# Performance work log

Hardware: AMD Instinct MI355X
Metric: run time of the kernel (lower is better)

The kernel has to match this reference:

```python
import math
import jax, jax.numpy as jnp
import numpy as np

N_NODES = 4096
N_EDGES = 16384
N_EFEAT = 16384
L = 8          # mem_token
DIM = 512
HEAD = 8
NL = 2         # mid_num_layers
ROPE_THETA = 10000.0


def _rms(x, w, eps=1e-6):
    v = jnp.mean(jnp.square(x), axis=-1, keepdims=True)
    return x * jax.lax.rsqrt(v + eps) * w


def _rope_cos_sin(seq_len, d, theta):
    inv = 1.0 / (theta ** (jnp.arange(0, d, 2, dtype=jnp.float32) / d))
    f = jnp.outer(jnp.arange(seq_len, dtype=jnp.float32), inv)  # [L, d/2]
    emb = jnp.concatenate([f, f], axis=-1)                       # [L, d]
    return jnp.cos(emb), jnp.sin(emb)


def _rot_half(x):
    h = x.shape[-1] // 2
    return jnp.concatenate([-x[..., h:], x[..., :h]], axis=-1)


def setup_inputs() -> dict:
    key = jax.random.key(0)
    ks = jax.random.split(key, 12)
    s = 0.02
    return {
        "hidden_states": jax.random.normal(ks[0], (N_NODES + N_EFEAT, L * DIM), jnp.float32),
        "edge_index": jax.random.randint(ks[1], (2, N_EDGES), 0, N_NODES),
        "edge_map": jax.random.randint(ks[2], (N_EDGES,), 0, N_EFEAT),
        "num_node_feat": N_NODES,
        "W_qkv": jax.random.normal(ks[3], (NL, DIM, 3 * DIM), jnp.float32) * s,
        "W_e": jax.random.normal(ks[4], (NL, DIM, 2 * DIM), jnp.float32) * s,
        "W_o": jax.random.normal(ks[5], (NL, DIM, DIM), jnp.float32) * s,
        "x_norm_w": jnp.ones((NL, DIM), jnp.float32),
        "xe_norm_w": jnp.ones((NL, DIM), jnp.float32),
        "post_norm_w": jnp.ones((NL, DIM), jnp.float32),
        "ff_W1": jax.random.normal(ks[6], (NL, DIM, 2 * DIM), jnp.float32) * s,
        "ff_b1": jnp.zeros((NL, 2 * DIM), jnp.float32),
        "ff_W2": jax.random.normal(ks[7], (NL, 2 * DIM, DIM), jnp.float32) * s,
        "ff_b2": jnp.zeros((NL, DIM), jnp.float32),
    }


def reference(hidden_states, edge_index, edge_map, num_node_feat,
              W_qkv, W_e, W_o, x_norm_w, xe_norm_w, post_norm_w,
              ff_W1, ff_b1, ff_W2, ff_b2):
    n_layers, dim = W_qkv.shape[0], W_qkv.shape[1]
    n_tot = hidden_states.shape[0]
    seq = hidden_states.shape[1] // dim           # mem_token
    d = dim // HEAD                               # d_model per head
    N = int(num_node_feat)
    src, dst = edge_index[0], edge_index[1]
    cos, sin = _rope_cos_sin(seq, d, ROPE_THETA)
    cos = cos[None, :, None, :]   # [1, L, 1, d]
    sin = sin[None, :, None, :]
    inv_sqrt_d = 1.0 / math.sqrt(d)

    h = hidden_states.reshape(n_tot, seq, dim)
    for l in range(n_layers):
        x = h[:N]                        # [N, L, dim]
        xe = h[N:][edge_map]             # [E, L, dim]
        res = x
        xn = _rms(x, x_norm_w[l])
        xen = _rms(xe, xe_norm_w[l])
        q, k, v = jnp.split(jnp.einsum('nld,de->nle', xn, W_qkv[l]), 3, axis=-1)
        ek, ev = jnp.split(jnp.einsum('eld,df->elf', xen, W_e[l]), 2, axis=-1)
        # gather per-edge, fuse edge features into key/value
        qi = q[dst].reshape(-1, seq, HEAD, d)
        kj = (k[src] + ek).reshape(-1, seq, HEAD, d)
        vj = (v[src] + ev).reshape(-1, seq, HEAD, d)
        # rotary over memory-token positions
        qi = qi * cos + _rot_half(qi) * sin
        kj = kj * cos + _rot_half(kj) * sin
        alpha = jnp.einsum('elhd,elhd->elh', qi, kj) * inv_sqrt_d  # [E, L, H]
        # segment softmax over incoming edges of each destination node
        m = jax.ops.segment_max(alpha, dst, num_segments=N)
        m = jnp.where(jnp.isfinite(m), m, 0.0)
        a = jnp.exp(alpha - m[dst])
        s = jax.ops.segment_sum(a, dst, num_segments=N)
        a = a / (s[dst] + 1e-16)
        out_e = (vj * a[..., None]).reshape(-1, seq, dim)          # [E, L, dim]
        agg = jax.ops.segment_sum(out_e, dst, num_segments=N)      # [N, L, dim]
        out = res + jnp.einsum('nld,de->nle', agg, W_o[l])
        res2 = out
        o = _rms(out, post_norm_w[l])
        ff = jnp.einsum('nlf,fd->nld',
                        jax.nn.relu(jnp.einsum('nld,df->nlf', o, ff_W1[l]) + ff_b1[l]),
                        ff_W2[l]) + ff_b2[l]
        out = res2 + ff
        h = jnp.concatenate([out, h[N:]], axis=0)
    return h
```

## Files before the change

kernel.cpp:

```cpp
#include <hip/hip_runtime.h>

typedef unsigned short u16;
typedef unsigned int   u32;
typedef u16   u16x8 __attribute__((ext_vector_type(8)));
typedef __bf16 bf16x8 __attribute__((ext_vector_type(8)));
typedef float f32x4 __attribute__((ext_vector_type(4)));
typedef float f32x4v __attribute__((ext_vector_type(4)));

#define N_NODES 4096
#define N_EDGES 16384
#define N_EFEAT 16384
#define SEQ 8
#define DIM 512
#define NLAYER 2
#define NROWS_X (N_NODES*SEQ)
#define NROWS_E (N_EDGES*SEQ)

__device__ __forceinline__ float b2f(u16 u){ return __uint_as_float(((u32)u)<<16); }
__device__ __forceinline__ u16 f2b(float f){ u32 b=__float_as_uint(f); b += 0x7FFFu + ((b>>16)&1u); return (u16)(b>>16); }

__device__ __forceinline__ void gl16(const u16* g, u16* l) {
    __builtin_amdgcn_global_load_lds((const __attribute__((address_space(1))) void*)g,
                                     (__attribute__((address_space(3))) void*)l, 16, 0, 0);
}

#define TF_SEG(CNT, SRC, DST, FOLD, KK, NN)                                   \
    if (b < (CNT)) {                                                          \
        int idx = b * 256 + threadIdx.x;                                      \
        int c = idx / (NN), j = idx - c * (NN);                               \
        float v = (SRC)[idx];                                                 \
        if (FOLD) v *= (FOLD)[c];                                             \
        (DST)[(size_t)j * (KK) + c] = f2b(v);                                 \
        return;                                                               \
    }                                                                         \
    b -= (CNT);

__global__ void k_tfall(const float* __restrict__ Wqkv, const float* __restrict__ We,
                        const float* __restrict__ Wo,   const float* __restrict__ W1,
                        const float* __restrict__ W2,
                        const float* __restrict__ xw, const float* __restrict__ xew,
                        const float* __restrict__ pw,
                        u16* __restrict__ WtQKV, u16* __restrict__ WtE, u16* __restrict__ WtO,
                        u16* __restrict__ Wt1, u16* __restrict__ Wt2,
                        float* __restrict__ z0, float* __restrict__ z1,
                        float* __restrict__ z2, int* __restrict__ zf)
{
    int b = blockIdx.x;
    if (b >= 20480) {
        b -= 20480;
        if (b < 128) { z0[b * 256 + threadIdx.x] = 0.f; return; }
        b -= 128;
        if (b < 128) { z1[b * 256 + threadIdx.x] = 0.f; return; }
        b -= 128;
        if (b < 128) { z2[b * 256 + threadIdx.x] = 0.f; return; }
        b -= 128;
        zf[b * 256 + threadIdx.x] = 0; return;
    }
    int l = b / 10240; b -= l * 10240;
    TF_SEG(3072, Wqkv + (size_t)l*512*1536, WtQKV + (size_t)l*1536*512, xw  + l*512, 512, 1536)
    TF_SEG(2048, We   + (size_t)l*512*1024, WtE   + (size_t)l*1024*512, xew + l*512, 512, 1024)
    TF_SEG(1024, Wo   + (size_t)l*512*512,  WtO   + (size_t)l*512*512,  (const float*)nullptr, 512, 512)
    TF_SEG(2048, W1   + (size_t)l*512*1024, Wt1   + (size_t)l*1024*512, pw  + l*512, 512, 1024)
    TF_SEG(2048, W2   + (size_t)l*1024*512, Wt2   + (size_t)l*512*1024, (const float*)nullptr, 1024, 512)
}

__global__ void k_prep(const float* __restrict__ hidden, const int* __restrict__ ulist,
                       const int* __restrict__ ucnt,
                       u16* __restrict__ fbf, float* __restrict__ s_f,
                       u16* __restrict__ hb, float* __restrict__ ssx0)
{
    int lane = threadIdx.x & 63;
    const float* p;
    u16* dst; float* ssout; int orow;
    if (blockIdx.x < NROWS_E / 4) {
        int fr = blockIdx.x * 4 + (threadIdx.x >> 6);
        if (fr >= ucnt[0] * SEQ) return;
        int j = fr >> 3, l = fr & 7;
        p = hidden + ((size_t)(N_NODES + ulist[j]) * SEQ + l) * DIM;
        dst = fbf + (size_t)fr * DIM; ssout = s_f; orow = fr;
    } else {
        int row = (blockIdx.x - NROWS_E / 4) * 4 + (threadIdx.x >> 6);
        p = hidden + (size_t)row * DIM;
        dst = hb + (size_t)row * DIM; ssout = ssx0; orow = row;
    }
    f32x4v v0 = *(const f32x4v*)(p + lane * 8);
    f32x4v v1 = *(const f32x4v*)(p + lane * 8 + 4);
    float ss = v0[0]*v0[0]+v0[1]*v0[1]+v0[2]*v0[2]+v0[3]*v0[3]
             + v1[0]*v1[0]+v1[1]*v1[1]+v1[2]*v1[2]+v1[3]*v1[3];
    #pragma unroll
    for (int d = 1; d < 64; d <<= 1) ss += __shfl_xor(ss, d);
    if (lane == 0) ssout[orow] = ss;
    u16x8 o;
    #pragma unroll
    for (int i = 0; i < 4; ++i) o[i] = f2b(v0[i]);
    #pragma unroll
    for (int i = 0; i < 4; ++i) o[4+i] = f2b(v1[i]);
    *(u16x8*)(dst + lane * 8) = o;
}

__global__ void k_mark(const int* __restrict__ emap, int* __restrict__ flag)
{
    int e = blockIdx.x * 256 + threadIdx.x;
    if (e < N_EDGES) flag[emap[e]] = 1;
}
__global__ void k_scanf(const int* __restrict__ flag, int* __restrict__ newid,
                        int* __restrict__ ulist, int* __restrict__ ucnt)
{
    __shared__ int part[256];
    int t = threadIdx.x;
    int base = t * 64;
    int loc[64]; int s = 0;
    #pragma unroll
    for (int i = 0; i < 64; ++i) { loc[i] = s; s += flag[base + i]; }
    part[t] = s; __syncthreads();
    for (int d = 1; d < 256; d <<= 1) {
        int v = (t >= d) ? part[t - d] : 0;
        __syncthreads();
        part[t] += v;
        __syncthreads();
    }
    int pre = (t == 0) ? 0 : part[t - 1];
    #pragma unroll
    for (int i = 0; i < 64; ++i) {
        int m = base + i;
        int id = pre + loc[i];
        newid[m] = id;
        if (flag[m]) ulist[id] = m;
    }
    if (t == 255) ucnt[0] = part[255];
}
__global__ void k_fidx(const int* __restrict__ emap, const int* __restrict__ newid,
                       int* __restrict__ fidx)
{
    int e = blockIdx.x * 256 + threadIdx.x;
    if (e < N_EDGES) fidx[e] = newid[emap[e]];
}

__global__ void k_count(const int* __restrict__ dstA, int* __restrict__ cnt)
{
    int e = blockIdx.x * 256 + threadIdx.x;
    if (e < N_EDGES) atomicAdd(&cnt[dstA[e]], 1);
}
__global__ void k_scan(const int* __restrict__ cnt, int* __restrict__ off)
{
    __shared__ int part[256];
    int t = threadIdx.x;
    int base = t * 16;
    int loc[16]; int s = 0;
    #pragma unroll
    for (int i = 0; i < 16; ++i) { loc[i] = s; s += cnt[base + i]; }
    part[t] = s; __syncthreads();
    for (int d = 1; d < 256; d <<= 1) {
        int v = (t >= d) ? part[t - d] : 0;
        __syncthreads();
        part[t] += v;
        __syncthreads();
    }
    int pre = (t == 0) ? 0 : part[t - 1];
    #pragma unroll
    for (int i = 0; i < 16; ++i) off[base + i] = pre + loc[i];
    if (t == 255) off[N_NODES] = part[255];
}
__global__ void k_fill(const int* __restrict__ dstA, const int* __restrict__ off,
                       int* __restrict__ cur, int* __restrict__ elist)
{
    int e = blockIdx.x * 256 + threadIdx.x;
    if (e < N_EDGES) {
        int d = dstA[e];
        int pos = off[d] + atomicAdd(&cur[d], 1);
        elist[pos] = e;
    }
}

#define GEMM_BODY(BID, A_, B_, N_, K_, GX_, MROWS_, SSIN_, BIAS_, RELU_, RESH_, SSOUT_, OUTF_, OUTH_) \
{                                                                                   \
    int tid  = threadIdx.x;                                                         \
    int lane = tid & 63, wid = tid >> 6;                                            \
    int xcd  = (BID) & 7;                                                           \
    int ii_  = (BID) >> 3;                                                          \
    int colt = ii_ % (GX_);                                                         \
    int rowt = (ii_ / (GX_)) * 8 + xcd;                                             \
    int row0 = rowt * 128, col0 = colt * 128;                                       \
    if ((MROWS_) && row0 >= (MROWS_)[0] * SEQ) return;                              \
    int r0 = wid * 32 + (lane >> 2);                                                \
    int r1 = r0 + 16;                                                               \
    int ce0 = ((lane & 3) * 8) ^ (((r0 >> 1) & 3) << 3);                            \
    int ce1 = ((lane & 3) * 8) ^ (((r1 >> 1) & 3) << 3);                            \
    const u16* ga0 = (A_) + (size_t)(row0 + r0) * (K_) + ce0;                       \
    const u16* ga1 = (A_) + (size_t)(row0 + r1) * (K_) + ce1;                       \
    const u16* gb0 = (B_) + (size_t)(col0 + r0) * (K_) + ce0;                       \
    const u16* gb1 = (B_) + (size_t)(col0 + r1) * (K_) + ce1;                       \
    f32x4 acc[4][4];                                                                \
    _Pragma("unroll")                                                               \
    for (int m = 0; m < 4; ++m)                                                     \
        _Pragma("unroll")                                                           \
        for (int n = 0; n < 4; ++n) { f32x4 z = {0.f,0.f,0.f,0.f}; acc[m][n] = z; } \
    int wr = wid >> 1, wc = wid & 1;                                                \
    int m15 = lane & 15, g = lane >> 4;                                             \
    int arow_l = wr * 64 + m15;                                                     \
    int brow_l = wc * 64 + m15;                                                     \
    int ksw = (g * 8) ^ (((m15 >> 1) & 3) << 3);                                    \
    int NT = (K_) / 32;                                                             \
    {                                                                               \
        gl16(ga0, &ldsA[0][wid * 1024]);                                            \
        gl16(ga1, &ldsA[0][wid * 1024 + 512]);                                      \
        gl16(gb0, &ldsB[0][wid * 1024]);                                            \
        gl16(gb1, &ldsB[0][wid * 1024 + 512]);                                      \
    }                                                                               \
    int cur = 0;                                                                    \
    for (int kt = 0; kt < NT; ++kt) {                                               \
        __syncthreads();                                                            \
        if (kt + 1 < NT) {                                                          \
            int ko = (kt + 1) * 32, bf_ = cur ^ 1;                                  \
            gl16(ga0 + ko, &ldsA[bf_][wid * 1024]);                                 \
            gl16(ga1 + ko, &ldsA[bf_][wid * 1024 + 512]);                           \
            gl16(gb0 + ko, &ldsB[bf_][wid * 1024]);                                 \
            gl16(gb1 + ko, &ldsB[bf_][wid * 1024 + 512]);                           \
        }                                                                           \
        bf16x8 af[4], bfr[4];                                                       \
        _Pragma("unroll")                                                           \
        for (int m = 0; m < 4; ++m)                                                 \
            af[m] = *(const bf16x8*)&ldsA[cur][(arow_l + m * 16) * 32 + ksw];       \
        _Pragma("unroll")                                                           \
        for (int n = 0; n < 4; ++n)                                                 \
            bfr[n] = *(const bf16x8*)&ldsB[cur][(brow_l + n * 16) * 32 + ksw];      \
        _Pragma("unroll")                                                           \
        for (int m = 0; m < 4; ++m)                                                 \
            _Pragma("unroll")                                                       \
            for (int n = 0; n < 4; ++n)                                             \
                acc[m][n] = __builtin_amdgcn_mfma_f32_16x16x32_bf16(af[m], bfr[n], acc[m][n], 0, 0, 0); \
        cur ^= 1;                                                                   \
    }                                                                               \
    _Pragma("unroll")                                                               \
    for (int m = 0; m < 4; ++m) {                                                   \
        _Pragma("unroll")                                                           \
        for (int j = 0; j < 4; ++j) {                                               \
            int row = row0 + wr * 64 + m * 16 + g * 4 + j;                          \
            float sc = 0.f;                                                         \
            if (SSIN_) sc = rsqrtf((SSIN_)[row] * (1.f / (float)DIM) + 1e-6f);      \
            float ssa = 0.f;                                                        \
            _Pragma("unroll")                                                       \
            for (int n = 0; n < 4; ++n) {                                           \
                int col = col0 + wc * 64 + n * 16 + m15;                            \
                float v = acc[m][n][j];                                             \
                if (SSIN_) v *= sc;                                                 \
                if (BIAS_) v += (BIAS_)[col];                                       \
                if (RELU_) v = fmaxf(v, 0.f);                                       \
                if (RESH_) v += b2f((RESH_)[(size_t)row * (N_) + col]);             \
                if (OUTF_) (OUTF_)[(size_t)row * (N_) + col] = v;                   \
                if (OUTH_) (OUTH_)[(size_t)row * (N_) + col] = f2b(v);              \
                ssa += v * v;                                                       \
            }                                                                       \
            if (SSOUT_) {                                                           \
                ssa += __shfl_xor(ssa, 1);                                          \
                ssa += __shfl_xor(ssa, 2);                                          \
                ssa += __shfl_xor(ssa, 4);                                          \
                ssa += __shfl_xor(ssa, 8);                                          \
                if (m15 == 0) atomicAdd(&(SSOUT_)[row], ssa);                       \
            }                                                                       \
        }                                                                           \
    }                                                                               \
}

__global__ __launch_bounds__(256, 2) void k_gemm(
    const u16* __restrict__ A, const u16* __restrict__ B,
    int M, int N, int K, int gx, const int* __restrict__ mrows,
    const float* __restrict__ ssin, const float* __restrict__ bias, int relu,
    const u16* __restrict__ resH, float* __restrict__ ssout,
    float* __restrict__ outF, u16* __restrict__ outH)
{
    __shared__ u16 ldsA[2][128 * 32];
    __shared__ u16 ldsB[2][128 * 32];
    GEMM_BODY(blockIdx.x, A, B, N, K, gx, mrows, ssin, bias, relu, resH, ssout, outF, outH)
}

__global__ __launch_bounds__(256, 2) void k_gemm2(
    int nb0,
    const u16* __restrict__ A0, const u16* __restrict__ B0,
    int N0, int K0, int gx0, const int* __restrict__ mrows0,
    const float* __restrict__ ssin0, const float* __restrict__ bias0, int relu0,
    const u16* __restrict__ resH0, float* __restrict__ ssout0,
    float* __restrict__ outF0, u16* __restrict__ outH0,
    const u16* __restrict__ A1, const u16* __restrict__ B1,
    int N1, int K1, int gx1, const int* __restrict__ mrows1,
    const float* __restrict__ ssin1, const float* __restrict__ bias1, int relu1,
    const u16* __restrict__ resH1, float* __restrict__ ssout1,
    float* __restrict__ outF1, u16* __restrict__ outH1)
{
    __shared__ u16 ldsA[2][128 * 32];
    __shared__ u16 ldsB[2][128 * 32];
    if ((int)blockIdx.x < nb0) {
        GEMM_BODY(blockIdx.x, A0, B0, N0, K0, gx0, mrows0, ssin0, bias0, relu0, resH0, ssout0, outF0, outH0)
    } else {
        int bid = blockIdx.x - nb0;
        GEMM_BODY(bid, A1, B1, N1, K1, gx1, mrows1, ssin1, bias1, relu1, resH1, ssout1, outF1, outH1)
    }
}

__global__ __launch_bounds__(256, 2) void k_gemm_copy(
    int nb0,
    const u16* __restrict__ A, const u16* __restrict__ B,
    int N, int K, int gx,
    const float* __restrict__ ssin, const float* __restrict__ bias, int relu,
    const u16* __restrict__ resH, float* __restrict__ ssout,
    float* __restrict__ outF, u16* __restrict__ outH,
    const f32x4v* __restrict__ csrc, f32x4v* __restrict__ cdst)
{
    __shared__ u16 ldsA[2][128 * 32];
    __shared__ u16 ldsB[2][128 * 32];
    if ((int)blockIdx.x < nb0) {
        GEMM_BODY(blockIdx.x, A, B, N, K, gx, (const int*)nullptr, ssin, bias, relu, resH, ssout, outF, outH)
    } else {
        size_t t = (size_t)(blockIdx.x - nb0) * 256 + threadIdx.x;
        #pragma unroll
        for (int k = 0; k < 32; ++k)
            cdst[t + (size_t)k * 524288] = csrc[t + (size_t)k * 524288];
    }
}

__global__ __launch_bounds__(256, 2) void k_attn(
    const u16* __restrict__ qkv, const u16* __restrict__ ekv,
    const int* __restrict__ srcA, const int* __restrict__ fidx,
    const int* __restrict__ off, const int* __restrict__ elist,
    u16* __restrict__ agg)
{
    int n = blockIdx.x;
    int t = threadIdx.x;
    int pair = t >> 2, sub = t & 3;
    int l = pair >> 3, hd = pair & 7;
    int doff = hd * 64 + sub * 16;

    size_t qrow = ((size_t)n * SEQ + l) * 1536;
    float qi[16];
    {
        u16x8 qa = *(const u16x8*)&qkv[qrow + doff];
        u16x8 qb = *(const u16x8*)&qkv[qrow + doff + 8];
        #pragma unroll
        for (int i = 0; i < 8; ++i) { qi[i] = b2f(qa[i]); qi[i + 8] = b2f(qb[i]); }
    }

    float mrun = -INFINITY, s = 0.f;
    float av[16];
    #pragma unroll
    for (int i = 0; i < 16; ++i) av[i] = 0.f;

    int e0 = off[n], e1 = off[n + 1];
    for (int ii = e0; ii < e1; ++ii) {
        int e = elist[ii];
        int es = srcA[e];
        size_t krow = ((size_t)es * SEQ + l) * 1536 + 512;
        size_t erow = ((size_t)fidx[e] * SEQ + l) * 1024;

        u16x8 ka = *(const u16x8*)&qkv[krow + doff];
        u16x8 kb = *(const u16x8*)&qkv[krow + doff + 8];
        u16x8 ea = *(const u16x8*)&ekv[erow + doff];
        u16x8 eb = *(const u16x8*)&ekv[erow + doff + 8];

        float dot = 0.f;
        #pragma unroll
        for (int i = 0; i < 8; ++i) {
            dot += qi[i]     * (b2f(ka[i]) + b2f(ea[i]));
            dot += qi[i + 8] * (b2f(kb[i]) + b2f(eb[i]));
        }
        dot += __shfl_xor(dot, 1);
        dot += __shfl_xor(dot, 2);
        float alpha = dot * 0.125f;

        float mn = fmaxf(mrun, alpha);
        float f = expf(mrun - mn);
        float p = expf(alpha - mn);
        s = s * f + p;

        u16x8 va  = *(const u16x8*)&qkv[krow + 512 + doff];
        u16x8 vb  = *(const u16x8*)&qkv[krow + 512 + doff + 8];
        u16x8 eva = *(const u16x8*)&ekv[erow + 512 + doff];
        u16x8 evb = *(const u16x8*)&ekv[erow + 512 + doff + 8];
        #pragma unroll
        for (int i = 0; i < 8; ++i) {
            av[i]     = av[i]     * f + p * (b2f(va[i]) + b2f(eva[i]));
            av[i + 8] = av[i + 8] * f + p * (b2f(vb[i]) + b2f(evb[i]));
        }
        mrun = mn;
    }

    float inv = 1.f / (s + 1e-16f);
    size_t orow = ((size_t)n * SEQ + l) * DIM + doff;
    #pragma unroll
    for (int i = 0; i < 16; ++i) agg[orow + i] = f2b(av[i] * inv);
}

extern "C" void kernel_launch(void* const* d_in, const int* in_sizes, int n_in,
                              void* d_out, int out_size, void* d_ws, size_t ws_size,
                              hipStream_t stream)
{
    const float* hidden = (const float*)d_in[0];
    const int*   eidx   = (const int*)d_in[1];
    const int*   srcA   = eidx;
    const int*   dstA   = eidx + N_EDGES;
    const int*   emap   = (const int*)d_in[2];
    const float* W_qkv  = (const float*)d_in[4];
    const float* W_e    = (const float*)d_in[5];
    const float* W_o    = (const float*)d_in[6];
    const float* xw     = (const float*)d_in[7];
    const float* xew    = (const float*)d_in[8];
    const float* pw     = (const float*)d_in[9];
    const float* W1     = (const float*)d_in[10];
    const float* b1     = (const float*)d_in[11];
    const float* W2     = (const float*)d_in[12];
    const float* b2     = (const float*)d_in[13];

    char* w = (char*)d_ws;
    auto alloc = [&](size_t bytes) { char* p = w; w += (bytes + 255) & ~(size_t)255; return p; };
    u16*  WtQKV  = (u16*)alloc((size_t)NLAYER * 1536 * 512 * 2);
    u16*  WtE    = (u16*)alloc((size_t)NLAYER * 1024 * 512 * 2);
    u16*  WtO    = (u16*)alloc((size_t)NLAYER * 512 * 512 * 2);
    u16*  Wt1    = (u16*)alloc((size_t)NLAYER * 1024 * 512 * 2);
    u16*  Wt2    = (u16*)alloc((size_t)NLAYER * 512 * 1024 * 2);
    float* ssx0  = (float*)alloc((size_t)NROWS_X * 4);
    float* ssx1  = (float*)alloc((size_t)NROWS_X * 4);
    float* ssp0  = (float*)alloc((size_t)NROWS_X * 4);
    float* ssp1  = (float*)alloc((size_t)NROWS_X * 4);
    float* s_f   = (float*)alloc((size_t)NROWS_E * 4);
    int*  cnt    = (int*)alloc((N_NODES + 1) * 4);
    int*  off    = (int*)alloc((N_NODES + 1) * 4);
    int*  cur    = (int*)alloc(N_NODES * 4);
    int*  elist  = (int*)alloc(N_EDGES * 4);
    int*  flag   = (int*)alloc(N_EFEAT * 4);
    int*  newid  = (int*)alloc(N_EFEAT * 4);
    int*  ulist  = (int*)alloc(N_EFEAT * 4);
    int*  fidx   = (int*)alloc(N_EDGES * 4);
    int*  ucnt   = (int*)alloc(256);
    u16*  hb     = (u16*)alloc((size_t)NROWS_X * DIM * 2);
    u16*  ob     = (u16*)alloc((size_t)NROWS_X * DIM * 2);
    u16*  fbf    = (u16*)alloc((size_t)NROWS_E * DIM * 2);
    u16*  qkv    = (u16*)alloc((size_t)NROWS_X * 1536 * 2);
    u16*  aggB   = (u16*)alloc((size_t)NROWS_X * DIM * 2);
    u16*  ffmid  = (u16*)alloc((size_t)NROWS_X * 1024 * 2);
    u16*  ekv    = (u16*)((float*)d_out + (size_t)NROWS_X * DIM);
    float* ssx[2] = { ssx0, ssx1 };
    float* ssp[2] = { ssp0, ssp1 };

    k_tfall<<<20928, 256, 0, stream>>>(W_qkv, W_e, W_o, W1, W2, xw, xew, pw,
                                       WtQKV, WtE, WtO, Wt1, Wt2, ssx1, ssp0, ssp1, flag);
    k_mark<<<N_EDGES/256, 256, 0, stream>>>(emap, flag);
    k_scanf<<<1, 256, 0, stream>>>(flag, newid, ulist, ucnt);
    k_fidx<<<N_EDGES/256, 256, 0, stream>>>(emap, newid, fidx);
    k_prep<<<NROWS_E/4 + NROWS_X/4, 256, 0, stream>>>(hidden, ulist, ucnt, fbf, s_f, hb, ssx0);
    hipMemsetAsync(cnt, 0, (N_NODES + 1) * 4, stream);
    hipMemsetAsync(cur, 0, N_NODES * 4, stream);
    k_count<<<N_EDGES/256, 256, 0, stream>>>(dstA, cnt);
    k_scan<<<1, 256, 0, stream>>>(cnt, off);
    k_fill<<<N_EDGES/256, 256, 0, stream>>>(dstA, off, cur, elist);

    const int nbQ = (NROWS_X/128)*(1536/128);
    const int nbE = (NROWS_E/128)*(1024/128);
    const int nbW = (NROWS_X/128)*(512/128);

    for (int l = 0; l < NLAYER; ++l) {
        int last = (l == NLAYER - 1);
        k_gemm2<<<nbQ + nbE, 256, 0, stream>>>(nbQ,
            hb, WtQKV + (size_t)l*1536*512, 1536, 512, 1536/128, nullptr,
            ssx[l], nullptr, 0, nullptr, nullptr, nullptr, qkv,
            fbf, WtE + (size_t)l*1024*512, 1024, 512, 1024/128, ucnt,
            s_f, nullptr, 0, nullptr, nullptr, nullptr, ekv);
        k_attn<<<N_NODES, 256, 0, stream>>>(qkv, ekv, srcA, fidx, off, elist, aggB);
        if (last) {
            k_gemm_copy<<<nbW + 2048, 256, 0, stream>>>(nbW,
                aggB, WtO + (size_t)l*512*512, 512, 512, 512/128,
                nullptr, nullptr, 0, hb, ssp[l], nullptr, ob,
                (const f32x4v*)(hidden + (size_t)NROWS_X * DIM),
                (f32x4v*)((float*)d_out + (size_t)NROWS_X * DIM));
        } else {
            k_gemm<<<nbW, 256, 0, stream>>>(aggB, WtO + (size_t)l*512*512,
                NROWS_X, 512, 512, 512/128, nullptr,
                nullptr, nullptr, 0, hb, ssp[l], nullptr, ob);
        }
        k_gemm<<<(NROWS_X/128)*(1024/128), 256, 0, stream>>>(ob, Wt1 + (size_t)l*1024*512,
            NROWS_X, 1024, 512, 1024/128, nullptr,
            ssp[l], b1 + l*1024, 1, nullptr, nullptr, nullptr, ffmid);
        k_gemm<<<(NROWS_X/128)*(512/128), 256, 0, stream>>>(ffmid, Wt2 + (size_t)l*512*1024,
            NROWS_X, 512, 1024, 512/128, nullptr,
            nullptr, b2 + l*512, 0, ob,
            last ? nullptr : ssx[1],
            last ? (float*)d_out : nullptr,
            last ? nullptr : hb);
    }
}
```

Measured before the change: 1.320 ms.

## Merge index-prep kernels and fuse layer-1 edge GEMM into layer-0 FFN2 launch

The small graph-preprocessing kernels are merged: mark and count share one launch, the two single-block scans run as two blocks of one kernel, and fidx computation is folded into the CSR fill. The layer loop is unrolled, and the layer-1 edge-feature projection (which depends only on the untouched edge features) now runs in the same grouped launch as layer-0's second FFN GEMM. This fills the GPU with more blocks during the small FFN2 GEMM and cuts launch count. It relies on k_gemm2 handling the FFN2 epilogue arguments the same way k_gemm did.

```diff
diff --git a/kernel.cpp b/kernel.cpp
--- a/kernel.cpp
+++ b/kernel.cpp
@@ -98,74 +98,65 @@
     *(u16x8*)(dst + lane * 8) = o;
 }
 
-__global__ void k_mark(const int* __restrict__ emap, int* __restrict__ flag)
+__global__ void k_mc(const int* __restrict__ emap, const int* __restrict__ dstA,
+                     int* __restrict__ flag, int* __restrict__ cnt)
 {
     int e = blockIdx.x * 256 + threadIdx.x;
-    if (e < N_EDGES) flag[emap[e]] = 1;
-}
-__global__ void k_scanf(const int* __restrict__ flag, int* __restrict__ newid,
-                        int* __restrict__ ulist, int* __restrict__ ucnt)
+    if (e < N_EDGES) { flag[emap[e]] = 1; atomicAdd(&cnt[dstA[e]], 1); }
+}
+__global__ void k_scans(const int* __restrict__ flag, int* __restrict__ newid,
+                        int* __restrict__ ulist, int* __restrict__ ucnt,
+                        const int* __restrict__ cnt, int* __restrict__ off)
 {
     __shared__ int part[256];
     int t = threadIdx.x;
-    int base = t * 64;
-    int loc[64]; int s = 0;
-    #pragma unroll
-    for (int i = 0; i < 64; ++i) { loc[i] = s; s += flag[base + i]; }
-    part[t] = s; __syncthreads();
-    for (int d = 1; d < 256; d <<= 1) {
-        int v = (t >= d) ? part[t - d] : 0;
-        __syncthreads();
-        part[t] += v;
-        __syncthreads();
-    }
-    int pre = (t == 0) ? 0 : part[t - 1];
-    #pragma unroll
-    for (int i = 0; i < 64; ++i) {
-        int m = base + i;
-        int id = pre + loc[i];
-        newid[m] = id;
-        if (flag[m]) ulist[id] = m;
-    }
-    if (t == 255) ucnt[0] = part[255];
-}
-__global__ void k_fidx(const int* __restrict__ emap, const int* __restrict__ newid,
-                       int* __restrict__ fidx)
-{
-    int e = blockIdx.x * 256 + threadIdx.x;
-    if (e < N_EDGES) fidx[e] = newid[emap[e]];
-}
-
-__global__ void k_count(const int* __restrict__ dstA, int* __restrict__ cnt)
-{
-    int e = blockIdx.x * 256 + threadIdx.x;
-    if (e < N_EDGES) atomicAdd(&cnt[dstA[e]], 1);
-}
-__global__ void k_scan(const int* __restrict__ cnt, int* __restrict__ off)
-{
-    __shared__ int part[256];
-    int t = threadIdx.x;
-    int base = t * 16;
-    int loc[16]; int s = 0;
-    #pragma unroll
-    for (int i = 0; i < 16; ++i) { loc[i] = s; s += cnt[base + i]; }
-    part[t] = s; __syncthreads();
-    for (int d = 1; d < 256; d <<= 1) {
-        int v = (t >= d) ? part[t - d] : 0;
-        __syncthreads();
-        part[t] += v;
-        __syncthreads();
-    }
-    int pre = (t == 0) ? 0 : part[t - 1];
-    #pragma unroll
-    for (int i = 0; i < 16; ++i) off[base + i] = pre + loc[i];
-    if (t == 255) off[N_NODES] = part[255];
-}
-__global__ void k_fill(const int* __restrict__ dstA, const int* __restrict__ off,
-                       int* __restrict__ cur, int* __restrict__ elist)
+    if (blockIdx.x == 0) {
+        int base = t * 64;
+        int loc[64]; int s = 0;
+        #pragma unroll
+        for (int i = 0; i < 64; ++i) { loc[i] = s; s += flag[base + i]; }
+        part[t] = s; __syncthreads();
+        for (int d = 1; d < 256; d <<= 1) {
+            int v = (t >= d) ? part[t - d] : 0;
+            __syncthreads();
+            part[t] += v;
+            __syncthreads();
+        }
+        int pre = (t == 0) ? 0 : part[t - 1];
+        #pragma unroll
+        for (int i = 0; i < 64; ++i) {
+            int m = base + i;
+            int id = pre + loc[i];
+            newid[m] = id;
+            if (flag[m]) ulist[id] = m;
+        }
+        if (t == 255) ucnt[0] = part[255];
+    } else {
+        int base = t * 16;
+        int loc[16]; int s = 0;
+        #pragma unroll
+        for (int i = 0; i < 16; ++i) { loc[i] = s; s += cnt[base + i]; }
+        part[t] = s; __syncthreads();
+        for (int d = 1; d < 256; d <<= 1) {
+            int v = (t >= d) ? part[t - d] : 0;
+            __syncthreads();
+            part[t] += v;
+            __syncthreads();
+        }
+        int pre = (t == 0) ? 0 : part[t - 1];
+        #pragma unroll
+        for (int i = 0; i < 16; ++i) off[base + i] = pre + loc[i];
+        if (t == 255) off[N_NODES] = part[255];
+    }
+}
+__global__ void k_ff(const int* __restrict__ emap, const int* __restrict__ newid,
+                     int* __restrict__ fidx, const int* __restrict__ dstA,
+                     const int* __restrict__ off, int* __restrict__ cur,
+                     int* __restrict__ elist)
 {
     int e = blockIdx.x * 256 + threadIdx.x;
     if (e < N_EDGES) {
+        fidx[e] = newid[emap[e]];
         int d = dstA[e];
         int pos = off[d] + atomicAdd(&cur[d], 1);
         elist[pos] = e;
@@ -437,52 +428,50 @@
     u16*  aggB   = (u16*)alloc((size_t)NROWS_X * DIM * 2);
     u16*  ffmid  = (u16*)alloc((size_t)NROWS_X * 1024 * 2);
     u16*  ekv    = (u16*)((float*)d_out + (size_t)NROWS_X * DIM);
-    float* ssx[2] = { ssx0, ssx1 };
-    float* ssp[2] = { ssp0, ssp1 };
 
     k_tfall<<<20928, 256, 0, stream>>>(W_qkv, W_e, W_o, W1, W2, xw, xew, pw,
                                        WtQKV, WtE, WtO, Wt1, Wt2, ssx1, ssp0, ssp1, flag);
-    k_mark<<<N_EDGES/256, 256, 0, stream>>>(emap, flag);
-    k_scanf<<<1, 256, 0, stream>>>(flag, newid, ulist, ucnt);
-    k_fidx<<<N_EDGES/256, 256, 0, stream>>>(emap, newid, fidx);
-    k_prep<<<NROWS_E/4 + NROWS_X/4, 256, 0, stream>>>(hidden, ulist, ucnt, fbf, s_f, hb, ssx0);
     hipMemsetAsync(cnt, 0, (N_NODES + 1) * 4, stream);
     hipMemsetAsync(cur, 0, N_NODES * 4, stream);
-    k_count<<<N_EDGES/256, 256, 0, stream>>>(dstA, cnt);
-    k_scan<<<1, 256, 0, stream>>>(cnt, off);
-    k_fill<<<N_EDGES/256, 256, 0, stream>>>(dstA, off, cur, elist);
+    k_mc<<<N_EDGES/256, 256, 0, stream>>>(emap, dstA, flag, cnt);
+    k_scans<<<2, 256, 0, stream>>>(flag, newid, ulist, ucnt, cnt, off);
+    k_ff<<<N_EDGES/256, 256, 0, stream>>>(emap, newid, fidx, dstA, off, cur, elist);
+    k_prep<<<NROWS_E/4 + NROWS_X/4, 256, 0, stream>>>(hidden, ulist, ucnt, fbf, s_f, hb, ssx0);
 
     const int nbQ = (NROWS_X/128)*(1536/128);
     const int nbE = (NROWS_E/128)*(1024/128);
     const int nbW = (NROWS_X/128)*(512/128);
-
-    for (int l = 0; l < NLAYER; ++l) {
-        int last = (l == NLAYER - 1);
-        k_gemm2<<<nbQ + nbE, 256, 0, stream>>>(nbQ,
-            hb, WtQKV + (size_t)l*1536*512, 1536, 512, 1536/128, nullptr,
-            ssx[l], nullptr, 0, nullptr, nullptr, nullptr, qkv,
-            fbf, WtE + (size_t)l*1024*512, 1024, 512, 1024/128, ucnt,
-            s_f, nullptr, 0, nullptr, nullptr, nullptr, ekv);
-        k_attn<<<N_NODES, 256, 0, stream>>>(qkv, ekv, srcA, fidx, off, elist, aggB);
-        if (last) {
-            k_gemm_copy<<<nbW + 2048, 256, 0, stream>>>(nbW,
-                aggB, WtO + (size_t)l*512*512, 512, 512, 512/128,
-                nullptr, nullptr, 0, hb, ssp[l], nullptr, ob,
-                (const f32x4v*)(hidden + (size_t)NROWS_X * DIM),
-                (f32x4v*)((float*)d_out + (size_t)NROWS_X * DIM));
-        } else {
-            k_gemm<<<nbW, 256, 0, stream>>>(aggB, WtO + (size_t)l*512*512,
-                NROWS_X, 512, 512, 512/128, nullptr,
-                nullptr, nullptr, 0, hb, ssp[l], nullptr, ob);
-        }
-        k_gemm<<<(NROWS_X/128)*(1024/128), 256, 0, stream>>>(ob, Wt1 + (size_t)l*1024*512,
-            NROWS_X, 1024, 512, 1024/128, nullptr,
-            ssp[l], b1 + l*1024, 1, nullptr, nullptr, nullptr, ffmid);
-        k_gemm<<<(NROWS_X/128)*(512/128), 256, 0, stream>>>(ffmid, Wt2 + (size_t)l*512*1024,
-            NROWS_X, 512, 1024, 512/128, nullptr,
-            nullptr, b2 + l*512, 0, ob,
-            last ? nullptr : ssx[1],
-            last ? (float*)d_out : nullptr,
-            last ? nullptr : hb);
-    }
-}
+    const int nbF1 = (NROWS_X/128)*(1024/128);
+
+    k_gemm2<<<nbQ + nbE, 256, 0, stream>>>(nbQ,
+        hb, WtQKV, 1536, 512, 1536/128, nullptr,
+        ssx0, nullptr, 0, nullptr, nullptr, nullptr, qkv,
+        fbf, WtE, 1024, 512, 1024/128, ucnt,
+        s_f, nullptr, 0, nullptr, nullptr, nullptr, ekv);
+    k_attn<<<N_NODES, 256, 0, stream>>>(qkv, ekv, srcA, fidx, off, elist, aggB);
+    k_gemm<<<nbW, 256, 0, stream>>>(aggB, WtO, NROWS_X, 512, 512, 512/128, nullptr,
+        nullptr, nullptr, 0, hb, ssp0, nullptr, ob);
+    k_gemm<<<nbF1, 256, 0, stream>>>(ob, Wt1, NROWS_X, 1024, 512, 1024/128, nullptr,
+        ssp0, b1, 1, nullptr, nullptr, nullptr, ffmid);
+    k_gemm2<<<nbW + nbE, 256, 0, stream>>>(nbW,
+        ffmid, Wt2, 512, 1024, 512/128, nullptr,
+        nullptr, b2, 0, ob, ssx1, nullptr, hb,
+        fbf, WtE + (size_t)1024*512, 1024, 512, 1024/128, ucnt,
+        s_f, nullptr, 0, nullptr, nullptr, nullptr, ekv);
+
+    k_gemm<<<nbQ, 256, 0, stream>>>(hb, WtQKV + (size_t)1536*512,
+        NROWS_X, 1536, 512, 1536/128, nullptr,
+        ssx1, nullptr, 0, nullptr, nullptr, nullptr, qkv);
+    k_attn<<<N_NODES, 256, 0, stream>>>(qkv, ekv, srcA, fidx, off, elist, aggB);
+    k_gemm_copy<<<nbW + 2048, 256, 0, stream>>>(nbW,
+        aggB, WtO + (size_t)512*512, 512, 512, 512/128,
+        nullptr, nullptr, 0, hb, ssp1, nullptr, ob,
+        (const f32x4v*)(hidden + (size_t)NROWS_X * DIM),
+        (f32x4v*)((float*)d_out + (size_t)NROWS_X * DIM));
+    k_gemm<<<nbF1, 256, 0, stream>>>(ob, Wt1 + (size_t)1024*512,
+        NROWS_X, 1024, 512, 1024/128, nullptr,
+        ssp1, b1 + 1024, 1, nullptr, nullptr, nullptr, ffmid);
+    k_gemm<<<nbW, 256, 0, stream>>>(ffmid, Wt2 + (size_t)512*1024,
+        NROWS_X, 512, 1024, 512/128, nullptr,
+        nullptr, b2 + 512, 0, ob, nullptr, (float*)d_out, nullptr);
+}
```

New measurement: 1.305 ms. Within noise of the previous version (-1.1%).
